# Kernel optimization log

Hardware: AMD Instinct MI355X
Metric: run time of the kernel (lower is better)

Reference implementation:

```python
import jax, jax.numpy as jnp
import numpy as np

EPS = 1e-5
GROUPS = 8


def setup_inputs() -> dict:
    key = jax.random.key(0)
    ks = jax.random.split(key, 7)
    B, C, H, W = 4, 512, 64, 64
    x = jax.random.normal(ks[0], (B, C, H, W), dtype=jnp.float32)
    gn_w = jax.random.normal(ks[1], (C,), dtype=jnp.float32) * 0.02 + 1.0
    gn_b = jax.random.normal(ks[2], (C,), dtype=jnp.float32) * 0.02
    # 1x1 convs stored as [out, in] matrices
    qkv_w = jax.random.normal(ks[3], (3 * C, C), dtype=jnp.float32) * (C ** -0.5)
    qkv_b = jax.random.normal(ks[4], (3 * C,), dtype=jnp.float32) * 0.02
    proj_w = jax.random.normal(ks[5], (C, C), dtype=jnp.float32) * (C ** -0.5)
    proj_b = jax.random.normal(ks[6], (C,), dtype=jnp.float32) * 0.02
    return {"x": x, "gn_w": gn_w, "gn_b": gn_b, "qkv_w": qkv_w,
            "qkv_b": qkv_b, "proj_w": proj_w, "proj_b": proj_b}


def _group_norm(x, w, b):
    B, C, H, W = x.shape
    xg = x.reshape(B, GROUPS, C // GROUPS, H, W)
    mu = jnp.mean(xg, axis=(2, 3, 4), keepdims=True)
    var = jnp.var(xg, axis=(2, 3, 4), keepdims=True)
    xn = ((xg - mu) * jax.lax.rsqrt(var + EPS)).reshape(B, C, H, W)
    return xn * w[None, :, None, None] + b[None, :, None, None]


def reference(x, gn_w, gn_b, qkv_w, qkv_b, proj_w, proj_b):
    B, C, H, W = x.shape
    N = H * W
    scale = C ** (-0.5)
    h = _group_norm(x, gn_w, gn_b)
    # 1x1 conv -> [B, 3C, N]
    qkv = jnp.einsum('oc,bcn->bon', qkv_w, h.reshape(B, C, N)) + qkv_b[None, :, None]
    q, k, v = jnp.split(qkv, 3, axis=1)  # each [B, C, N]
    # scores[b, n, m] = sum_c q[b,c,n] * k[b,c,m]
    attn = jax.nn.softmax(jnp.einsum('bcn,bcm->bnm', q, k) * scale, axis=-1)
    # out[b,c,n] = sum_m v[b,c,m] * attn[b,n,m]   (v @ attn^T)
    hout = jnp.einsum('bcm,bnm->bcn', v, attn)
    proj = jnp.einsum('oc,bcn->bon', proj_w, hout) + proj_b[None, :, None]
    return x + proj.reshape(B, C, H, W)
```

## Files before the change

### kernel.cpp

```cpp
#include <hip/hip_runtime.h>
#include <math.h>

#define SCALE 0.044194173824159216f
#define QI 28.22222222f
#define K8SCL ((4.5f/127.0f)*(4.5f/127.0f)*SCALE)
#define PSCL 0.49609375f
#define VSCL 0.035433070866141736f

typedef __bf16 bf16x8 __attribute__((ext_vector_type(8)));
typedef float  f32x4  __attribute__((ext_vector_type(4)));
typedef int    i32x4  __attribute__((ext_vector_type(4)));
typedef unsigned int u32;

__device__ __forceinline__ void gload16(const void* g, void* l) {
    __builtin_amdgcn_global_load_lds(
        (const __attribute__((address_space(1))) u32*)g,
        (__attribute__((address_space(3))) u32*)l, 16, 0, 0);
}

__global__ __launch_bounds__(256) void gn_part(const float* __restrict__ x,
                                               float* __restrict__ part) {
    int gi = blockIdx.x >> 4, sl = blockIdx.x & 15;
    const float4* p = (const float4*)(x + (size_t)gi * 64 * 4096) + (size_t)sl * 4096;
    float s = 0.f, ss = 0.f;
    #pragma unroll 4
    for (int i = threadIdx.x; i < 4096; i += 256) {
        float4 v = p[i];
        s  += v.x + v.y + v.z + v.w;
        ss += v.x*v.x + v.y*v.y + v.z*v.z + v.w*v.w;
    }
    __shared__ float rs[256], rss[256];
    rs[threadIdx.x] = s; rss[threadIdx.x] = ss;
    __syncthreads();
    for (int o = 128; o > 0; o >>= 1) {
        if (threadIdx.x < o) { rs[threadIdx.x] += rs[threadIdx.x+o]; rss[threadIdx.x] += rss[threadIdx.x+o]; }
        __syncthreads();
    }
    if (threadIdx.x == 0) {
        part[blockIdx.x*2 + 0] = rs[0];
        part[blockIdx.x*2 + 1] = rss[0];
    }
}

__global__ __launch_bounds__(64) void gn_fin(const float* __restrict__ part,
                                             float* __restrict__ stats) {
    int t = threadIdx.x;
    if (t < 32) {
        float s = 0.f, ss = 0.f;
        #pragma unroll
        for (int i = 0; i < 16; ++i) { s += part[(t*16+i)*2]; ss += part[(t*16+i)*2+1]; }
        float inv = 1.0f / (float)(64 * 4096);
        float mu  = s * inv;
        float var = ss * inv - mu * mu;
        stats[t*2 + 0] = mu;
        stats[t*2 + 1] = rsqrtf(var + 1e-5f);
    }
}

__global__ __launch_bounds__(256) void gn_apply_t(const float* __restrict__ x,
                                                  const float* __restrict__ stats,
                                                  const float* __restrict__ gw,
                                                  const float* __restrict__ gb,
                                                  __bf16* __restrict__ hT) {
    __shared__ __bf16 tile[64][88];
    int b = blockIdx.z, c0 = blockIdx.y * 64, n0 = blockIdx.x * 64;
    int t = threadIdx.x;
    float mu  = stats[(b*8 + blockIdx.y)*2];
    float rsg = stats[(b*8 + blockIdx.y)*2 + 1];
    int c = t >> 2, ns = t & 3;
    float a = gw[c0+c] * rsg;
    float d = gb[c0+c] - mu * a;
    const float* xr = x + ((size_t)b*512 + c0 + c)*4096 + n0 + ns*16;
    #pragma unroll
    for (int e4 = 0; e4 < 4; ++e4) {
        float4 v = *(const float4*)(xr + e4*4);
        tile[ns*16 + e4*4 + 0][c] = (__bf16)(v.x*a + d);
        tile[ns*16 + e4*4 + 1][c] = (__bf16)(v.y*a + d);
        tile[ns*16 + e4*4 + 2][c] = (__bf16)(v.z*a + d);
        tile[ns*16 + e4*4 + 3][c] = (__bf16)(v.w*a + d);
    }
    __syncthreads();
    int n = t >> 2, cs = t & 3;
    __bf16* dst = hT + ((size_t)b*4096 + n0 + n)*512 + c0 + cs*16;
    *(uint4*)(dst)     = *(const uint4*)(&tile[n][cs*16]);
    *(uint4*)(dst + 8) = *(const uint4*)(&tile[n][cs*16 + 8]);
}

__global__ __launch_bounds__(256) void wconv2(const float* __restrict__ qw,
                                              const float* __restrict__ pwsrc,
                                              __bf16* __restrict__ dst) {
    int i = (blockIdx.x*256 + threadIdx.x) * 4;
    const float* src = (i < 786432) ? (qw + i) : (pwsrc + (i - 786432));
    float4 v = *(const float4*)src;
    dst[i+0] = (__bf16)v.x; dst[i+1] = (__bf16)v.y;
    dst[i+2] = (__bf16)v.z; dst[i+3] = (__bf16)v.w;
}

template<int MODE>
__global__ __launch_bounds__(256) void mm128(
        const __bf16* __restrict__ A, int lda, size_t sA,
        const __bf16* __restrict__ B, int ldb, size_t sB,
        int Kdim,
        const float* __restrict__ bias,
        const float* __restrict__ res, size_t sR,
        void* __restrict__ out, int ldo, size_t sO) {
    __shared__ __bf16 As[3][128][32];
    __shared__ __bf16 Bs[3][128][32];

    const int t = threadIdx.x, w = t >> 6, l = t & 63;
    const int l15 = l & 15, lq = l >> 4;
    const int bz = blockIdx.z;

    const int gx = gridDim.x;
    int lin = blockIdx.y * gx + blockIdx.x;
    {
        const int nwg = gx * gridDim.y;
        const int qn = nwg >> 3, rn = nwg & 7;
        const int xcd = lin & 7, idx = lin >> 3;
        const int base = (xcd < rn) ? xcd*(qn+1) : rn*(qn+1) + (xcd-rn)*qn;
        lin = base + idx;
    }
    const int j0 = (lin % gx) * 128;
    const int i0 = (lin / gx) * 128;

    const __bf16* Ab = A + sA*bz;
    const __bf16* Bb = B + sB*bz;
    const int rowblk = (w & 1)*64;
    const int colblk = (w >> 1)*64;

    const int slot0 = w*64 + l;
    const int rowS0 = slot0 >> 2;
    const int rowS1 = rowS0 + 64;
    const int csS   = (((slot0 & 3) ^ ((rowS0 >> 1) & 3))) * 8;
    const int off0  = (w*64)*16;
    const int off1  = (256 + w*64)*16;

    f32x4 acc[4][4];
    #pragma unroll
    for (int mr = 0; mr < 4; ++mr)
        #pragma unroll
        for (int nr = 0; nr < 4; ++nr)
            #pragma unroll
            for (int r = 0; r < 4; ++r) acc[mr][nr][r] = 0.f;

    auto STAGE = [&](int kc, int bi) {
        char* Ad = (char*)As[bi];
        char* Bd = (char*)Bs[bi];
        gload16(Ab + (size_t)(i0 + rowS0)*lda + kc + csS, Ad + off0);
        gload16(Ab + (size_t)(i0 + rowS1)*lda + kc + csS, Ad + off1);
        gload16(Bb + (size_t)(j0 + rowS0)*ldb + kc + csS, Bd + off0);
        gload16(Bb + (size_t)(j0 + rowS1)*ldb + kc + csS, Bd + off1);
    };

    const int rsw = (l15 >> 1) & 3;
    const int koff = (lq ^ rsw) << 4;

    const int nch = Kdim >> 5;
    STAGE(0, 0);
    STAGE(32, 1);

    for (int cc = 0; cc < nch; ++cc) {
        if (cc < nch - 1) asm volatile("s_waitcnt vmcnt(4)\n\ts_barrier" ::: "memory");
        else              asm volatile("s_waitcnt vmcnt(0)\n\ts_barrier" ::: "memory");

        const char* Ac = (const char*)As[cc % 3];
        const char* Bc = (const char*)Bs[cc % 3];
        bf16x8 av[4], bv[4];
        #pragma unroll
        for (int mr = 0; mr < 4; ++mr)
            av[mr] = *(const bf16x8*)(Ac + (rowblk + mr*16 + l15)*64 + koff);
        #pragma unroll
        for (int nr = 0; nr < 4; ++nr)
            bv[nr] = *(const bf16x8*)(Bc + (colblk + nr*16 + l15)*64 + koff);
        if (cc + 2 < nch) STAGE((cc + 2)*32, (cc + 2) % 3);
        #pragma unroll
        for (int mr = 0; mr < 4; ++mr)
            #pragma unroll
            for (int nr = 0; nr < 4; ++nr)
                acc[mr][nr] = __builtin_amdgcn_mfma_f32_16x16x32_bf16(av[mr], bv[nr], acc[mr][nr], 0, 0, 0);
    }

    #pragma unroll
    for (int mr = 0; mr < 4; ++mr)
        #pragma unroll
        for (int nr = 0; nr < 4; ++nr) {
            int col = j0 + colblk + nr*16 + l15;
            #pragma unroll
            for (int r = 0; r < 4; ++r) {
                int lrow = rowblk + mr*16 + lq*4 + r;
                int gi = i0 + lrow;
                float v = acc[mr][nr][r];
                if constexpr (MODE == 1) {
                    v += bias[gi];
                    int q = __float2int_rn(v * QI);
                    q = q < -127 ? -127 : (q > 127 ? 127 : q);
                    ((char*)out)[sO*bz + (size_t)gi*ldo + col] = (char)q;
                } else {
                    v += bias[gi] + res[sR*bz + (size_t)gi*ldo + col];
                    ((float*)out)[sO*bz + (size_t)gi*ldo + col] = v;
                }
            }
        }
}

template<int M> struct AccT { using T = f32x4; };
template<> struct AccT<4> { using T = i32x4; };
template<> struct AccT<5> { using T = i32x4; };

#define LDSB (98304 + 4096)
template<int MODE>
__global__ __launch_bounds__(512) void mm256(
        const void* __restrict__ A, int ldaB, size_t sAB,
        const void* __restrict__ B, int ldbB, size_t sBB,
        int Kbytes,
        const float* __restrict__ bias,
        void* __restrict__ out, int ldo, size_t sO,
        float* __restrict__ rowpart) {
    extern __shared__ char smem[];
    char*  Abase = smem;
    char*  Bbase = smem + 49152;
    float* redp  = (float*)(smem + 98304);

    const int t = threadIdx.x, w = t >> 6, l = t & 63;
    const int l15 = l & 15, lq = l >> 4;
    const int bz = (MODE == 4) ? (blockIdx.z >> 1) : blockIdx.z;
    const int kh = (MODE == 4) ? (blockIdx.z & 1) : 0;
    const size_t kbase = (size_t)kh * Kbytes;

    const int gx = gridDim.x;
    int lin = blockIdx.y * gx + blockIdx.x;
    {
        const int nwg = gx * gridDim.y;
        const int qn = nwg >> 3, rn = nwg & 7;
        const int xcd = lin & 7, idx = lin >> 3;
        const int base = (xcd < rn) ? xcd*(qn+1) : rn*(qn+1) + (xcd-rn)*qn;
        lin = base + idx;
    }
    const int j0 = (lin % gx) * 256;
    const int i0 = (lin / gx) * 256;

    const char* Ab = (const char*)A + sAB*bz + kbase;
    const char* Bb = (const char*)B + sBB*bz + kbase;
    const int wr = w & 1;
    const int wc = w >> 1;

    const int slot0 = w*64 + l;
    const int rowS0 = slot0 >> 2;
    const int rowS1 = rowS0 + 128;
    const int csS   = (((slot0 & 3) ^ ((rowS0 >> 1) & 3))) * 16;
    const int off0  = (w*64)*16;
    const int off1  = (512 + w*64)*16;

    typename AccT<MODE>::T acc[8][4];
    #pragma unroll
    for (int mr = 0; mr < 8; ++mr)
        #pragma unroll
        for (int nr = 0; nr < 4; ++nr)
            #pragma unroll
            for (int r = 0; r < 4; ++r) acc[mr][nr][r] = 0;

    auto STAGE = [&](int kc, int bi) {
        char* Ad = Abase + bi*16384;
        char* Bd = Bbase + bi*16384;
        gload16(Ab + (size_t)(i0 + rowS0)*ldaB + kc + csS, Ad + off0);
        gload16(Ab + (size_t)(i0 + rowS1)*ldaB + kc + csS, Ad + off1);
        gload16(Bb + (size_t)(j0 + rowS0)*ldbB + kc + csS, Bd + off0);
        gload16(Bb + (size_t)(j0 + rowS1)*ldbB + kc + csS, Bd + off1);
    };

    const int rsw = (l15 >> 1) & 3;
    const int koff = (lq ^ rsw) << 4;

    const int nch = Kbytes >> 6;
    STAGE(0, 0);
    STAGE(64, 1);

    for (int cc = 0; cc < nch; ++cc) {
        if (cc < nch - 1) asm volatile("s_waitcnt vmcnt(4)\n\ts_barrier" ::: "memory");
        else              asm volatile("s_waitcnt vmcnt(0)\n\ts_barrier" ::: "memory");

        const char* Ac = Abase + (cc % 3)*16384;
        const char* Bc = Bbase + (cc % 3)*16384;
        i32x4 araw[8], braw[4];
        #pragma unroll
        for (int mr = 0; mr < 8; ++mr)
            araw[mr] = *(const i32x4*)(Ac + (wr*128 + mr*16 + l15)*64 + koff);
        #pragma unroll
        for (int nr = 0; nr < 4; ++nr)
            braw[nr] = *(const i32x4*)(Bc + (wc*64 + nr*16 + l15)*64 + koff);
        if (cc + 2 < nch) STAGE((cc + 2)*64, (cc + 2) % 3);
        #pragma unroll
        for (int mr = 0; mr < 8; ++mr)
            #pragma unroll
            for (int nr = 0; nr < 4; ++nr) {
                if constexpr (MODE == 4 || MODE == 5) {
                    acc[mr][nr] = __builtin_amdgcn_mfma_i32_16x16x64_i8(
                        araw[mr], braw[nr], acc[mr][nr], 0, 0, 0);
                } else {
                    acc[mr][nr] = __builtin_amdgcn_mfma_f32_16x16x32_bf16(
                        __builtin_bit_cast(bf16x8, araw[mr]),
                        __builtin_bit_cast(bf16x8, braw[nr]), acc[mr][nr], 0, 0, 0);
                }
            }
    }

    if constexpr (MODE == 5) {
        const int jblk = j0 >> 8;
        float rpart[8][4];
        #pragma unroll
        for (int mr = 0; mr < 8; ++mr)
            #pragma unroll
            for (int r = 0; r < 4; ++r) rpart[mr][r] = 0.f;
        #pragma unroll
        for (int mr = 0; mr < 8; ++mr)
            #pragma unroll
            for (int nr = 0; nr < 4; ++nr) {
                int col = j0 + wc*64 + nr*16 + l15;
                #pragma unroll
                for (int r = 0; r < 4; ++r) {
                    int row = wr*128 + mr*16 + lq*4 + r;
                    float e = __expf((float)acc[mr][nr][r] * K8SCL);
                    int q = __float2int_rn(e * PSCL);
                    if (q > 127) q = 127;
                    ((char*)out)[sO*bz + (size_t)(i0 + row)*ldo + col] = (char)q;
                    rpart[mr][r] += (float)q;
                }
            }
        #pragma unroll
        for (int m = 1; m < 16; m <<= 1)
            #pragma unroll
            for (int mr = 0; mr < 8; ++mr)
                #pragma unroll
                for (int r = 0; r < 4; ++r)
                    rpart[mr][r] += __shfl_xor(rpart[mr][r], m);
        __syncthreads();
        if (l15 == 0) {
            #pragma unroll
            for (int mr = 0; mr < 8; ++mr)
                #pragma unroll
                for (int r = 0; r < 4; ++r)
                    redp[(wr*128 + mr*16 + lq*4 + r)*4 + wc] = rpart[mr][r];
        }
        __syncthreads();
        if (t < 256)
            rowpart[(size_t)bz*131072 + (size_t)jblk*4096 + i0 + t] =
                redp[t*4+0] + redp[t*4+1] + redp[t*4+2] + redp[t*4+3];
        return;
    }

    #pragma unroll
    for (int mr = 0; mr < 8; ++mr)
        #pragma unroll
        for (int nr = 0; nr < 4; ++nr) {
            int col = j0 + wc*64 + nr*16 + l15;
            #pragma unroll
            for (int r = 0; r < 4; ++r) {
                int lrow = wr*128 + mr*16 + lq*4 + r;
                if constexpr (MODE == 0) {
                    float v = (float)acc[mr][nr][r] + bias[col];
                    int q = __float2int_rn(v * QI);
                    q = q < -127 ? -127 : (q > 127 ? 127 : q);
                    char* qk = (char*)out + (size_t)bz*8388608;
                    size_t row = (size_t)(i0 + lrow);
                    char* p = (col < 512) ? (qk + row*512 + col)
                                          : (qk + 2097152 + row*512 + (col - 512));
                    *p = (char)q;
                } else {
                    __bf16* po = (__bf16*)out + sO*bz + (size_t)kh*2097152;
                    po[(size_t)(i0 + lrow)*ldo + col] = (__bf16)(float)acc[mr][nr][r];
                }
            }
        }
}

__global__ __launch_bounds__(256) void pv_reduce(const __bf16* __restrict__ part,
                                                 const float* __restrict__ rowpart,
                                                 __bf16* __restrict__ OT) {
    int b = blockIdx.y, r0 = blockIdx.x * 16;
    __shared__ float rs[16];
    int t = threadIdx.x;
    if (t < 16) {
        const float* rp = rowpart + (size_t)b*131072 + r0 + t;
        float s = 0.f;
        #pragma unroll
        for (int jb = 0; jb < 16; ++jb) s += rp[jb*4096];
        rs[t] = VSCL / s;
    }
    __syncthreads();
    int row = r0 + (t >> 4), cseg = (t & 15) * 32;
    const __bf16* p0 = part + (size_t)b*16777216 + (size_t)row*512 + cseg;
    const __bf16* p1 = p0 + 2097152;
    __bf16* o = OT + (size_t)b*2097152 + (size_t)row*512 + cseg;
    float sc = rs[t >> 4];
    #pragma unroll
    for (int g = 0; g < 4; ++g) {
        bf16x8 a = *(const bf16x8*)(p0 + g*8);
        bf16x8 bb = *(const bf16x8*)(p1 + g*8);
        bf16x8 r;
        #pragma unroll
        for (int e = 0; e < 8; ++e) r[e] = (__bf16)(((float)a[e] + (float)bb[e]) * sc);
        *(bf16x8*)(o + g*8) = r;
    }
}

extern "C" void kernel_launch(void* const* d_in, const int* in_sizes, int n_in,
                              void* d_out, int out_size, void* d_ws, size_t ws_size,
                              hipStream_t stream) {
    const float* x      = (const float*)d_in[0];
    const float* gn_w   = (const float*)d_in[1];
    const float* gn_b   = (const float*)d_in[2];
    const float* qkv_w  = (const float*)d_in[3];
    const float* qkv_b  = (const float*)d_in[4];
    const float* proj_w = (const float*)d_in[5];
    const float* proj_b = (const float*)d_in[6];

    char* w8 = (char*)d_ws;
    char*   v8buf = w8 + 33554432;
    __bf16* OT   = (__bf16*)(w8 + 50331648);
    __bf16* wq   = (__bf16*)(w8 + 67108864);
    __bf16* pw   = (__bf16*)(w8 + 68681728);
    float*  rowpart = (float*)(w8 + 69206016);
    float*  part = (float*)(w8 + 71303168);
    float*  st   = (float*)(w8 + 71307264);
    const size_t baseP = 71307520ULL;
    __bf16* hT   = (__bf16*)(w8 + baseP);

    size_t avail = (ws_size > baseP) ? (ws_size - baseP) : 0;
    int cap = (int)(avail / 33554432ULL);
    if (cap < 1) cap = 1;
    if (cap > 4) cap = 4;

    hipFuncSetAttribute((const void*)mm256<0>,
                        hipFuncAttributeMaxDynamicSharedMemorySize, LDSB);
    hipFuncSetAttribute((const void*)mm256<4>,
                        hipFuncAttributeMaxDynamicSharedMemorySize, LDSB);
    hipFuncSetAttribute((const void*)mm256<5>,
                        hipFuncAttributeMaxDynamicSharedMemorySize, LDSB);

    wconv2<<<1024, 256, 0, stream>>>(qkv_w, proj_w, wq);
    gn_part<<<512, 256, 0, stream>>>(x, part);
    gn_fin<<<1, 64, 0, stream>>>(part, st);
    gn_apply_t<<<dim3(64, 8, 4), 256, 0, stream>>>(x, st, gn_w, gn_b, hT);

    mm256<0><<<dim3(4, 16, 4), 512, LDSB, stream>>>(
        hT, 1024, (size_t)4096*1024, wq, 1024, 0, 1024,
        qkv_b, w8, 0, 0, nullptr);
    mm128<1><<<dim3(32, 4, 4), 256, 0, stream>>>(
        wq + (size_t)1024*512, 512, 0, hT, 512, (size_t)4096*512, 512,
        qkv_b + 1024, nullptr, 0, v8buf, 4096, (size_t)512*4096);

    for (int b0 = 0; b0 < 4; b0 += cap) {
        int c = (4 - b0 < cap) ? (4 - b0) : cap;
        char* Pb = w8 + baseP + (size_t)b0*33554432;
        mm256<5><<<dim3(16, 16, c), 512, LDSB, stream>>>(
            w8 + (size_t)b0*8388608, 512, 8388608,
            w8 + (size_t)b0*8388608 + 2097152, 512, 8388608, 512,
            nullptr, Pb, 4096, 33554432,
            rowpart + (size_t)b0*131072);
        mm256<4><<<dim3(2, 16, c*2), 512, LDSB, stream>>>(
            Pb, 4096, 33554432,
            v8buf + (size_t)b0*2097152, 4096, 2097152, 2048,
            nullptr, Pb + 16777216, 512, 16777216,
            nullptr);
        pv_reduce<<<dim3(256, c), 256, 0, stream>>>(
            (const __bf16*)(Pb + 16777216), rowpart + (size_t)b0*131072,
            OT + (size_t)b0*2097152);
    }

    mm128<2><<<dim3(32, 4, 4), 256, 0, stream>>>(
        pw, 512, 0, OT, 512, (size_t)4096*512, 512,
        proj_b, x, (size_t)512*4096, (float*)d_out, 4096, (size_t)512*4096);
}
```

Before: 191.4 us.

## Switch GEMM K-loop to double-buffered 128-byte chunks with 8-way swizzle

Replaces the triple-buffered 64-byte K-chunk pipeline with a double-buffered pipeline of 128-byte K chunks. Each chunk is split into two MFMA sub-steps, the LDS swizzle widens to 8 columns, and LDS use grows to about 132KB. This halves the barriers per K and issues larger async loads, but the prefetch distance drops to one chunk and there is a full vmcnt(0) wait each iteration. Separately, the softmax exponent folds the probability scale into the exp argument via an FMA.

```diff
diff --git a/kernel.cpp b/kernel.cpp
--- a/kernel.cpp
+++ b/kernel.cpp
@@ -4,6 +4,7 @@
 #define SCALE 0.044194173824159216f
 #define QI 28.22222222f
 #define K8SCL ((4.5f/127.0f)*(4.5f/127.0f)*SCALE)
+#define LNPSCL (-0.70099024f)
 #define PSCL 0.49609375f
 #define VSCL 0.035433070866141736f
 
@@ -207,7 +208,7 @@
 template<> struct AccT<4> { using T = i32x4; };
 template<> struct AccT<5> { using T = i32x4; };
 
-#define LDSB (98304 + 4096)
+#define LDSB (131072 + 4096)
 template<int MODE>
 __global__ __launch_bounds__(512) void mm256(
         const void* __restrict__ A, int ldaB, size_t sAB,
@@ -218,8 +219,8 @@
         float* __restrict__ rowpart) {
     extern __shared__ char smem[];
     char*  Abase = smem;
-    char*  Bbase = smem + 49152;
-    float* redp  = (float*)(smem + 98304);
+    char*  Bbase = smem + 65536;
+    float* redp  = (float*)(smem + 131072);
 
     const int t = threadIdx.x, w = t >> 6, l = t & 63;
     const int l15 = l & 15, lq = l >> 4;
@@ -244,12 +245,14 @@
     const int wr = w & 1;
     const int wc = w >> 1;
 
-    const int slot0 = w*64 + l;
-    const int rowS0 = slot0 >> 2;
-    const int rowS1 = rowS0 + 128;
-    const int csS   = (((slot0 & 3) ^ ((rowS0 >> 1) & 3))) * 16;
-    const int off0  = (w*64)*16;
-    const int off1  = (512 + w*64)*16;
+    int srow[4], scs[4], soff[4];
+    #pragma unroll
+    for (int i = 0; i < 4; ++i) {
+        int s = i*512 + w*64 + l;
+        srow[i] = s >> 3;
+        scs[i]  = ((s & 7) ^ (srow[i] & 7)) * 16;
+        soff[i] = (i*512 + w*64) * 16;
+    }
 
     typename AccT<MODE>::T acc[8][4];
     #pragma unroll
@@ -260,48 +263,51 @@
             for (int r = 0; r < 4; ++r) acc[mr][nr][r] = 0;
 
     auto STAGE = [&](int kc, int bi) {
-        char* Ad = Abase + bi*16384;
-        char* Bd = Bbase + bi*16384;
-        gload16(Ab + (size_t)(i0 + rowS0)*ldaB + kc + csS, Ad + off0);
-        gload16(Ab + (size_t)(i0 + rowS1)*ldaB + kc + csS, Ad + off1);
-        gload16(Bb + (size_t)(j0 + rowS0)*ldbB + kc + csS, Bd + off0);
-        gload16(Bb + (size_t)(j0 + rowS1)*ldbB + kc + csS, Bd + off1);
+        char* Ad = Abase + bi*32768;
+        char* Bd = Bbase + bi*32768;
+        #pragma unroll
+        for (int i = 0; i < 4; ++i) {
+            gload16(Ab + (size_t)(i0 + srow[i])*ldaB + kc + scs[i], Ad + soff[i]);
+            gload16(Bb + (size_t)(j0 + srow[i])*ldbB + kc + scs[i], Bd + soff[i]);
+        }
     };
 
-    const int rsw = (l15 >> 1) & 3;
-    const int koff = (lq ^ rsw) << 4;
-
-    const int nch = Kbytes >> 6;
+    const int rsw = l15 & 7;
+    const int koffA[2] = { (lq ^ rsw) << 4, ((4 + lq) ^ rsw) << 4 };
+
+    const int nch = Kbytes >> 7;
     STAGE(0, 0);
-    STAGE(64, 1);
+    asm volatile("s_waitcnt vmcnt(0)\n\ts_barrier" ::: "memory");
 
     for (int cc = 0; cc < nch; ++cc) {
-        if (cc < nch - 1) asm volatile("s_waitcnt vmcnt(4)\n\ts_barrier" ::: "memory");
-        else              asm volatile("s_waitcnt vmcnt(0)\n\ts_barrier" ::: "memory");
-
-        const char* Ac = Abase + (cc % 3)*16384;
-        const char* Bc = Bbase + (cc % 3)*16384;
-        i32x4 araw[8], braw[4];
-        #pragma unroll
-        for (int mr = 0; mr < 8; ++mr)
-            araw[mr] = *(const i32x4*)(Ac + (wr*128 + mr*16 + l15)*64 + koff);
-        #pragma unroll
-        for (int nr = 0; nr < 4; ++nr)
-            braw[nr] = *(const i32x4*)(Bc + (wc*64 + nr*16 + l15)*64 + koff);
-        if (cc + 2 < nch) STAGE((cc + 2)*64, (cc + 2) % 3);
-        #pragma unroll
-        for (int mr = 0; mr < 8; ++mr)
-            #pragma unroll
-            for (int nr = 0; nr < 4; ++nr) {
-                if constexpr (MODE == 4 || MODE == 5) {
-                    acc[mr][nr] = __builtin_amdgcn_mfma_i32_16x16x64_i8(
-                        araw[mr], braw[nr], acc[mr][nr], 0, 0, 0);
-                } else {
-                    acc[mr][nr] = __builtin_amdgcn_mfma_f32_16x16x32_bf16(
-                        __builtin_bit_cast(bf16x8, araw[mr]),
-                        __builtin_bit_cast(bf16x8, braw[nr]), acc[mr][nr], 0, 0, 0);
+        if (cc + 1 < nch) STAGE((cc + 1)*128, (cc + 1) & 1);
+        const char* Ac = Abase + (cc & 1)*32768;
+        const char* Bc = Bbase + (cc & 1)*32768;
+        #pragma unroll
+        for (int f = 0; f < 2; ++f) {
+            const int ko = koffA[f];
+            i32x4 araw[8], braw[4];
+            #pragma unroll
+            for (int mr = 0; mr < 8; ++mr)
+                araw[mr] = *(const i32x4*)(Ac + (wr*128 + mr*16 + l15)*128 + ko);
+            #pragma unroll
+            for (int nr = 0; nr < 4; ++nr)
+                braw[nr] = *(const i32x4*)(Bc + (wc*64 + nr*16 + l15)*128 + ko);
+            #pragma unroll
+            for (int mr = 0; mr < 8; ++mr)
+                #pragma unroll
+                for (int nr = 0; nr < 4; ++nr) {
+                    if constexpr (MODE == 4 || MODE == 5) {
+                        acc[mr][nr] = __builtin_amdgcn_mfma_i32_16x16x64_i8(
+                            araw[mr], braw[nr], acc[mr][nr], 0, 0, 0);
+                    } else {
+                        acc[mr][nr] = __builtin_amdgcn_mfma_f32_16x16x32_bf16(
+                            __builtin_bit_cast(bf16x8, araw[mr]),
+                            __builtin_bit_cast(bf16x8, braw[nr]), acc[mr][nr], 0, 0, 0);
+                    }
                 }
-            }
+        }
+        if (cc + 1 < nch) asm volatile("s_waitcnt vmcnt(0)\n\ts_barrier" ::: "memory");
     }
 
     if constexpr (MODE == 5) {
@@ -319,8 +325,8 @@
                 #pragma unroll
                 for (int r = 0; r < 4; ++r) {
                     int row = wr*128 + mr*16 + lq*4 + r;
-                    float e = __expf((float)acc[mr][nr][r] * K8SCL);
-                    int q = __float2int_rn(e * PSCL);
+                    float e = __expf(fmaf((float)acc[mr][nr][r], K8SCL, LNPSCL));
+                    int q = __float2int_rn(e);
                     if (q > 127) q = 127;
                     ((char*)out)[sO*bz + (size_t)(i0 + row)*ldo + col] = (char)q;
                     rpart[mr][r] += (float)q;
```

New measurement: 190.7 us. About the same (-0.4%).
